# Optimization experiments

Hardware: AMD Instinct MI355X
Metric: run time of the kernel (lower is better)

Reference implementation:

```python
import jax, jax.numpy as jnp
import numpy as np

C = 64  # in_channels == out_channels (required by final view)

def setup_inputs() -> dict:
    key = jax.random.key(0)
    ks = jax.random.split(key, 7)
    x = jax.random.normal(ks[0], (2, C, 16, 16, 16), dtype=jnp.float32)
    s = 1.0 / np.sqrt(C)
    Wq = jax.random.uniform(ks[1], (C, C), jnp.float32, -s, s)
    bq = jax.random.uniform(ks[2], (C,), jnp.float32, -s, s)
    Wk = jax.random.uniform(ks[3], (C, C), jnp.float32, -s, s)
    bk = jax.random.uniform(ks[4], (C,), jnp.float32, -s, s)
    Wv = jax.random.uniform(ks[5], (C, C), jnp.float32, -s, s)
    bv = jax.random.uniform(ks[6], (C,), jnp.float32, -s, s)
    return {"x": x, "Wq": Wq, "bq": bq, "Wk": Wk, "bk": bk, "Wv": Wv, "bv": bv}

def _proj(x, W, b):
    # 1x1x1 Conv3d == per-voxel channel GEMM; x: [B,C,D,H,W]
    return jnp.einsum('oc,bcdhw->bodhw', W, x) + b[None, :, None, None, None]

def reference(x, Wq, bq, Wk, bk, Wv, bv):
    B, Cin, D, H, W = x.shape
    q = _proj(x, Wq, bq).reshape(B, C, -1)  # [B,C,N]
    k = _proj(x, Wk, bk).reshape(B, C, -1)
    v = _proj(x, Wv, bv).reshape(B, C, -1)
    # attention[b,i,j] = softmax_j(q_i . k_j); NOTE: unscaled, as in the source
    attn = jax.nn.softmax(jnp.einsum('bci,bcj->bij', q, k), axis=-1)
    out = jnp.einsum('bcj,bij->bci', v, attn)  # out_i = sum_j a_ij v_j
    return out.reshape(x.shape)
```

## Files before the change

kernel.cpp:

```cpp
#include <hip/hip_runtime.h>
#include <math.h>

#define CCH 64
#define NVOX 4096
#define NB 2
#define RS 72

typedef _Float16 f16x8 __attribute__((ext_vector_type(8)));
typedef float f32x4 __attribute__((ext_vector_type(4)));

__global__ __launch_bounds__(256) void qkv_proj(
    const float* __restrict__ x,
    const float* __restrict__ Wq, const float* __restrict__ bq,
    const float* __restrict__ Wk, const float* __restrict__ bk,
    const float* __restrict__ Wv, const float* __restrict__ bv,
    _Float16* __restrict__ qh, _Float16* __restrict__ kh, _Float16* __restrict__ vh)
{
    __shared__ float Ws[3 * 64 * 64];
    __shared__ float xs[64 * 32];
    const int t  = threadIdx.x;
    const int b  = blockIdx.x >> 7;
    const int i0 = (blockIdx.x & 127) * 32;

    {
        const float4* Wq4 = (const float4*)Wq;
        const float4* Wk4 = (const float4*)Wk;
        const float4* Wv4 = (const float4*)Wv;
        float4* Ws4 = (float4*)Ws;
#pragma unroll
        for (int s = 0; s < 4; ++s) {
            int idx = t + 256 * s;
            Ws4[idx]        = Wq4[idx];
            Ws4[1024 + idx] = Wk4[idx];
            Ws4[2048 + idx] = Wv4[idx];
        }
    }
    {
        int cc = t >> 2;
        int m0 = (t & 3) * 8;
        const float* src = x + ((b * CCH + cc) * NVOX) + i0 + m0;
#pragma unroll
        for (int s = 0; s < 8; ++s) xs[cc * 32 + m0 + s] = src[s];
    }
    __syncthreads();

    const int vox = t & 31;
    const int c0  = (t >> 5) * 8;

#pragma unroll
    for (int m = 0; m < 3; ++m) {
        const float* Wm  = &Ws[m * 4096];
        const float* bia = (m == 0) ? bq : (m == 1) ? bk : bv;
        float acc[8];
#pragma unroll
        for (int j = 0; j < 8; ++j) acc[j] = bia[c0 + j];
        for (int cc = 0; cc < 64; cc += 4) {
            float xv0 = xs[(cc + 0) * 32 + vox];
            float xv1 = xs[(cc + 1) * 32 + vox];
            float xv2 = xs[(cc + 2) * 32 + vox];
            float xv3 = xs[(cc + 3) * 32 + vox];
#pragma unroll
            for (int j = 0; j < 8; ++j) {
                float4 w = *(const float4*)&Wm[(c0 + j) * 64 + cc];
                acc[j] = fmaf(w.x, xv0, acc[j]);
                acc[j] = fmaf(w.y, xv1, acc[j]);
                acc[j] = fmaf(w.z, xv2, acc[j]);
                acc[j] = fmaf(w.w, xv3, acc[j]);
            }
        }
        if (m < 2) {
            f16x8 hv;
#pragma unroll
            for (int j = 0; j < 8; ++j) hv[j] = (_Float16)acc[j];
            _Float16* dst = ((m == 0) ? qh : kh) + ((b * NVOX) + i0 + vox) * CCH + c0;
            *(f16x8*)dst = hv;
        } else {
#pragma unroll
            for (int j = 0; j < 8; ++j)
                vh[(b * CCH + c0 + j) * NVOX + i0 + vox] = (_Float16)acc[j];
        }
    }
}

template <int SPLIT>
__global__ __launch_bounds__(256) void attn(
    const _Float16* __restrict__ qh, const _Float16* __restrict__ kh,
    const _Float16* __restrict__ vh,
    float* __restrict__ po,
    float* __restrict__ ml,
    float* __restrict__ out)
{
    __shared__ _Float16 qs [64 * RS];
    __shared__ _Float16 ksl[64 * RS];
    __shared__ _Float16 vsl[64 * RS];
    __shared__ _Float16 ps [4 * 16 * RS];
    __shared__ float    als[4 * 16];

    constexpr int LS = (SPLIT == 4) ? 2 : (SPLIT == 2) ? 1 : 0;
    const int t    = threadIdx.x;
    const int h    = blockIdx.x & (SPLIT - 1);
    const int tile = blockIdx.x >> LS;
    const int b    = tile >> 6;
    const int i0   = (tile & 63) * 64;

    const int lane = t & 63;
    const int w    = t >> 6;
    const int q4   = lane >> 4;
    const int n    = lane & 15;

    {
        int row = t >> 2, c0 = (t & 3) * 16;
        const float4* src = (const float4*)&qh[((b * NVOX) + i0 + row) * CCH + c0];
        *(float4*)&qs[row * RS + c0]     = src[0];
        *(float4*)&qs[row * RS + c0 + 8] = src[1];
    }

    f16x8 aq[2];
    float m_prev[4], l[4];
    f32x4 o[4];
#pragma unroll
    for (int r = 0; r < 4; ++r) { m_prev[r] = -1e30f; l[r] = 0.f; }
#pragma unroll
    for (int mt = 0; mt < 4; ++mt) o[mt] = (f32x4){0.f, 0.f, 0.f, 0.f};

    const int JT = 64 / SPLIT;
    for (int jt = 0; jt < JT; ++jt) {
        const int j0 = (h * JT + jt) * 64;
        __syncthreads();
        {
            int row = t >> 2, c0 = (t & 3) * 16;
            const float4* ks = (const float4*)&kh[((b * NVOX) + j0 + row) * CCH + c0];
            *(float4*)&ksl[row * RS + c0]     = ks[0];
            *(float4*)&ksl[row * RS + c0 + 8] = ks[1];
            const float4* vs = (const float4*)&vh[(b * CCH + row) * NVOX + j0 + c0];
            *(float4*)&vsl[row * RS + c0]     = vs[0];
            *(float4*)&vsl[row * RS + c0 + 8] = vs[1];
        }
        __syncthreads();

        if (jt == 0) {
#pragma unroll
            for (int ks = 0; ks < 2; ++ks)
                aq[ks] = *(const f16x8*)&qs[(w * 16 + n) * RS + ks * 32 + q4 * 8];
        }

        f32x4 s[4];
#pragma unroll
        for (int nt = 0; nt < 4; ++nt) s[nt] = (f32x4){0.f, 0.f, 0.f, 0.f};
#pragma unroll
        for (int ks = 0; ks < 2; ++ks) {
#pragma unroll
            for (int nt = 0; nt < 4; ++nt) {
                f16x8 bk = *(const f16x8*)&ksl[(nt * 16 + n) * RS + ks * 32 + q4 * 8];
                s[nt] = __builtin_amdgcn_mfma_f32_16x16x32_f16(aq[ks], bk, s[nt], 0, 0, 0);
            }
        }

        float p[4][4], alpha[4];
#pragma unroll
        for (int r = 0; r < 4; ++r) {
            float mx = fmaxf(fmaxf(s[0][r], s[1][r]), fmaxf(s[2][r], s[3][r]));
#pragma unroll
            for (int off = 1; off < 16; off <<= 1)
                mx = fmaxf(mx, __shfl_xor(mx, off, 64));
            float mn = fmaxf(m_prev[r], mx);
            float sum = 0.f;
#pragma unroll
            for (int nt = 0; nt < 4; ++nt) {
                p[nt][r] = __expf(s[nt][r] - mn);
                sum += p[nt][r];
            }
#pragma unroll
            for (int off = 1; off < 16; off <<= 1)
                sum += __shfl_xor(sum, off, 64);
            alpha[r]  = __expf(m_prev[r] - mn);
            l[r]      = l[r] * alpha[r] + sum;
            m_prev[r] = mn;
        }

#pragma unroll
        for (int nt = 0; nt < 4; ++nt)
#pragma unroll
            for (int r = 0; r < 4; ++r)
                ps[w * 16 * RS + (q4 * 4 + r) * RS + nt * 16 + n] = (_Float16)p[nt][r];
        if (n == 0)
            *(float4*)&als[w * 16 + q4 * 4] =
                make_float4(alpha[0], alpha[1], alpha[2], alpha[3]);
        __syncthreads();

        float a_i = als[w * 16 + n];
#pragma unroll
        for (int mt = 0; mt < 4; ++mt)
#pragma unroll
            for (int r = 0; r < 4; ++r) o[mt][r] *= a_i;

        f16x8 bp[2];
#pragma unroll
        for (int ks = 0; ks < 2; ++ks)
            bp[ks] = *(const f16x8*)&ps[w * 16 * RS + n * RS + ks * 32 + q4 * 8];
#pragma unroll
        for (int mt = 0; mt < 4; ++mt) {
#pragma unroll
            for (int ks = 0; ks < 2; ++ks) {
                f16x8 av = *(const f16x8*)&vsl[(mt * 16 + n) * RS + ks * 32 + q4 * 8];
                o[mt] = __builtin_amdgcn_mfma_f32_16x16x32_f16(av, bp[ks], o[mt], 0, 0, 0);
            }
        }
    }

    const int ig = i0 + w * 16 + n;
    if (SPLIT > 1) {
        const size_t base = ((size_t)(b * SPLIT + h) * 64) * NVOX;
#pragma unroll
        for (int mt = 0; mt < 4; ++mt)
#pragma unroll
            for (int r = 0; r < 4; ++r)
                po[base + (size_t)(mt * 16 + q4 * 4 + r) * NVOX + ig] = o[mt][r];
        if (n == 0) {
            const int mlbase = ((b * SPLIT + h) * NVOX + i0 + w * 16 + q4 * 4) * 2;
            *(float4*)&ml[mlbase]     = make_float4(m_prev[0], l[0], m_prev[1], l[1]);
            *(float4*)&ml[mlbase + 4] = make_float4(m_prev[2], l[2], m_prev[3], l[3]);
        }
    } else {
        if (n == 0)
            *(float4*)&als[w * 16 + q4 * 4] =
                make_float4(1.f / l[0], 1.f / l[1], 1.f / l[2], 1.f / l[3]);
        __syncthreads();
        float inv = als[w * 16 + n];
#pragma unroll
        for (int mt = 0; mt < 4; ++mt)
#pragma unroll
            for (int r = 0; r < 4; ++r)
                out[(size_t)(b * CCH + mt * 16 + q4 * 4 + r) * NVOX + ig] = o[mt][r] * inv;
    }
}

template <int SPLIT>
__global__ __launch_bounds__(256) void combine(
    const float* __restrict__ po, const float* __restrict__ ml,
    float* __restrict__ out)
{
    __shared__ float wls[SPLIT * 64];
    const int t  = threadIdx.x;
    const int b  = blockIdx.x >> 6;
    const int i0 = (blockIdx.x & 63) * 64;

    if (t < 64) {
        const int i = i0 + t;
        float mv[SPLIT], lv[SPLIT], M = -1e30f;
#pragma unroll
        for (int h = 0; h < SPLIT; ++h) {
            mv[h] = ml[((b * SPLIT + h) * NVOX + i) * 2 + 0];
            lv[h] = ml[((b * SPLIT + h) * NVOX + i) * 2 + 1];
            M = fmaxf(M, mv[h]);
        }
        float den = 0.f;
#pragma unroll
        for (int h = 0; h < SPLIT; ++h) den += lv[h] * __expf(mv[h] - M);
        const float inv = 1.0f / den;
#pragma unroll
        for (int h = 0; h < SPLIT; ++h) wls[h * 64 + t] = __expf(mv[h] - M) * inv;
    }
    __syncthreads();

    const int c  = t >> 2;
    const int iq = t & 3;
    float4 acc[4];
#pragma unroll
    for (int u = 0; u < 4; ++u) acc[u] = make_float4(0.f, 0.f, 0.f, 0.f);
#pragma unroll
    for (int h = 0; h < SPLIT; ++h) {
        const float4* src = (const float4*)&po[((size_t)(b * SPLIT + h) * 64 + c) * NVOX + i0 + iq * 16];
        const float*  wp  = &wls[h * 64 + iq * 16];
#pragma unroll
        for (int u = 0; u < 4; ++u) {
            float4 f = src[u];
            float4 wv = *(const float4*)&wp[u * 4];
            acc[u].x = fmaf(f.x, wv.x, acc[u].x);
            acc[u].y = fmaf(f.y, wv.y, acc[u].y);
            acc[u].z = fmaf(f.z, wv.z, acc[u].z);
            acc[u].w = fmaf(f.w, wv.w, acc[u].w);
        }
    }
    float4* dst = (float4*)&out[(size_t)(b * CCH + c) * NVOX + i0 + iq * 16];
#pragma unroll
    for (int u = 0; u < 4; ++u) dst[u] = acc[u];
}

extern "C" void kernel_launch(void* const* d_in, const int* in_sizes, int n_in,
                              void* d_out, int out_size, void* d_ws, size_t ws_size,
                              hipStream_t stream)
{
    const float* x  = (const float*)d_in[0];
    const float* Wq = (const float*)d_in[1];
    const float* bq = (const float*)d_in[2];
    const float* Wk = (const float*)d_in[3];
    const float* bk = (const float*)d_in[4];
    const float* Wv = (const float*)d_in[5];
    const float* bv = (const float*)d_in[6];
    float* out = (float*)d_out;

    _Float16* qh = (_Float16*)d_ws;
    _Float16* kh = qh + NB * NVOX * CCH;
    _Float16* vh = kh + NB * NVOX * CCH;
    float*    po = (float*)(vh + NB * NVOX * CCH);
    const size_t qkv_bytes = (size_t)3 * NB * NVOX * CCH * sizeof(_Float16);

    qkv_proj<<<NB * (NVOX / 32), 256, 0, stream>>>(x, Wq, bq, Wk, bk, Wv, bv, qh, kh, vh);

    const size_t need4 = qkv_bytes + (size_t)NB * 4 * (64 + 2) * NVOX * sizeof(float);
    const size_t need2 = qkv_bytes + (size_t)NB * 2 * (64 + 2) * NVOX * sizeof(float);

    if (ws_size >= need4) {
        float* ml = po + (size_t)NB * 4 * 64 * NVOX;
        attn<4><<<NB * 64 * 4, 256, 0, stream>>>(qh, kh, vh, po, ml, out);
        combine<4><<<NB * 64, 256, 0, stream>>>(po, ml, out);
    } else if (ws_size >= need2) {
        float* ml = po + (size_t)NB * 2 * 64 * NVOX;
        attn<2><<<NB * 64 * 2, 256, 0, stream>>>(qh, kh, vh, po, ml, out);
        combine<2><<<NB * 64, 256, 0, stream>>>(po, ml, out);
    } else {
        attn<1><<<NB * 64, 256, 0, stream>>>(qh, kh, vh, nullptr, nullptr, out);
    }
}
```

Before: 118.0 us.

## Transpose QK^T MFMA to keep P in registers and add split-8 path

The score MFMA is swapped to compute S^T, so each lane owns one query column. The softmax row max and sum then need only two cross-lane shuffles, and the probabilities can feed the PV MFMA (16x16x16) straight from registers. This removes the P and alpha shared-memory staging, an extra __syncthreads per tile, and the Q shared-memory staging. A SPLIT=8 variant is also added when the workspace allows, giving more blocks in exchange for more partial-output traffic in combine.

```diff
diff --git a/kernel.cpp b/kernel.cpp
--- a/kernel.cpp
+++ b/kernel.cpp
@@ -7,6 +7,7 @@
 #define RS 72
 
 typedef _Float16 f16x8 __attribute__((ext_vector_type(8)));
+typedef _Float16 f16x4 __attribute__((ext_vector_type(4)));
 typedef float f32x4 __attribute__((ext_vector_type(4)));
 
 __global__ __launch_bounds__(256) void qkv_proj(
@@ -90,13 +91,10 @@
     float* __restrict__ ml,
     float* __restrict__ out)
 {
-    __shared__ _Float16 qs [64 * RS];
     __shared__ _Float16 ksl[64 * RS];
     __shared__ _Float16 vsl[64 * RS];
-    __shared__ _Float16 ps [4 * 16 * RS];
-    __shared__ float    als[4 * 16];
-
-    constexpr int LS = (SPLIT == 4) ? 2 : (SPLIT == 2) ? 1 : 0;
+
+    constexpr int LS = (SPLIT == 8) ? 3 : (SPLIT == 4) ? 2 : (SPLIT == 2) ? 1 : 0;
     const int t    = threadIdx.x;
     const int h    = blockIdx.x & (SPLIT - 1);
     const int tile = blockIdx.x >> LS;
@@ -108,18 +106,15 @@
     const int q4   = lane >> 4;
     const int n    = lane & 15;
 
+    f16x8 aq[2];
     {
-        int row = t >> 2, c0 = (t & 3) * 16;
-        const float4* src = (const float4*)&qh[((b * NVOX) + i0 + row) * CCH + c0];
-        *(float4*)&qs[row * RS + c0]     = src[0];
-        *(float4*)&qs[row * RS + c0 + 8] = src[1];
-    }
-
-    f16x8 aq[2];
-    float m_prev[4], l[4];
+        const _Float16* qrow = qh + ((size_t)(b * NVOX) + i0 + w * 16 + n) * CCH + q4 * 8;
+        aq[0] = *(const f16x8*)(qrow);
+        aq[1] = *(const f16x8*)(qrow + 32);
+    }
+
+    float m_prev = -1e30f, l = 0.f;
     f32x4 o[4];
-#pragma unroll
-    for (int r = 0; r < 4; ++r) { m_prev[r] = -1e30f; l[r] = 0.f; }
 #pragma unroll
     for (int mt = 0; mt < 4; ++mt) o[mt] = (f32x4){0.f, 0.f, 0.f, 0.f};
 
@@ -129,21 +124,15 @@
         __syncthreads();
         {
             int row = t >> 2, c0 = (t & 3) * 16;
-            const float4* ks = (const float4*)&kh[((b * NVOX) + j0 + row) * CCH + c0];
+            const float4* ks = (const float4*)&kh[((size_t)(b * NVOX) + j0 + row) * CCH + c0];
             *(float4*)&ksl[row * RS + c0]     = ks[0];
             *(float4*)&ksl[row * RS + c0 + 8] = ks[1];
-            const float4* vs = (const float4*)&vh[(b * CCH + row) * NVOX + j0 + c0];
+            const float4* vs = (const float4*)&vh[((size_t)b * CCH + row) * NVOX + j0 + c0];
             *(float4*)&vsl[row * RS + c0]     = vs[0];
             *(float4*)&vsl[row * RS + c0 + 8] = vs[1];
         }
         __syncthreads();
 
-        if (jt == 0) {
-#pragma unroll
-            for (int ks = 0; ks < 2; ++ks)
-                aq[ks] = *(const f16x8*)&qs[(w * 16 + n) * RS + ks * 32 + q4 * 8];
-        }
-
         f32x4 s[4];
 #pragma unroll
         for (int nt = 0; nt < 4; ++nt) s[nt] = (f32x4){0.f, 0.f, 0.f, 0.f};
@@ -151,59 +140,52 @@
         for (int ks = 0; ks < 2; ++ks) {
 #pragma unroll
             for (int nt = 0; nt < 4; ++nt) {
-                f16x8 bk = *(const f16x8*)&ksl[(nt * 16 + n) * RS + ks * 32 + q4 * 8];
-                s[nt] = __builtin_amdgcn_mfma_f32_16x16x32_f16(aq[ks], bk, s[nt], 0, 0, 0);
+                f16x8 ak = *(const f16x8*)&ksl[(nt * 16 + n) * RS + ks * 32 + q4 * 8];
+                s[nt] = __builtin_amdgcn_mfma_f32_16x16x32_f16(ak, aq[ks], s[nt], 0, 0, 0);
             }
         }
 
-        float p[4][4], alpha[4];
-#pragma unroll
-        for (int r = 0; r < 4; ++r) {
-            float mx = fmaxf(fmaxf(s[0][r], s[1][r]), fmaxf(s[2][r], s[3][r]));
-#pragma unroll
-            for (int off = 1; off < 16; off <<= 1)
-                mx = fmaxf(mx, __shfl_xor(mx, off, 64));
-            float mn = fmaxf(m_prev[r], mx);
-            float sum = 0.f;
-#pragma unroll
-            for (int nt = 0; nt < 4; ++nt) {
+        float mx = -1e30f;
+#pragma unroll
+        for (int nt = 0; nt < 4; ++nt)
+#pragma unroll
+            for (int r = 0; r < 4; ++r) mx = fmaxf(mx, s[nt][r]);
+        mx = fmaxf(mx, __shfl_xor(mx, 16, 64));
+        mx = fmaxf(mx, __shfl_xor(mx, 32, 64));
+        const float mn = fmaxf(m_prev, mx);
+
+        float p[4][4], sum = 0.f;
+#pragma unroll
+        for (int nt = 0; nt < 4; ++nt)
+#pragma unroll
+            for (int r = 0; r < 4; ++r) {
                 p[nt][r] = __expf(s[nt][r] - mn);
                 sum += p[nt][r];
             }
-#pragma unroll
-            for (int off = 1; off < 16; off <<= 1)
-                sum += __shfl_xor(sum, off, 64);
-            alpha[r]  = __expf(m_prev[r] - mn);
-            l[r]      = l[r] * alpha[r] + sum;
-            m_prev[r] = mn;
-        }
-
+        sum += __shfl_xor(sum, 16, 64);
+        sum += __shfl_xor(sum, 32, 64);
+
+        const float alpha = __expf(m_prev - mn);
+        l = l * alpha + sum;
+        m_prev = mn;
+
+#pragma unroll
+        for (int mt = 0; mt < 4; ++mt)
+#pragma unroll
+            for (int r = 0; r < 4; ++r) o[mt][r] *= alpha;
+
+        f16x4 bp[4];
 #pragma unroll
         for (int nt = 0; nt < 4; ++nt)
 #pragma unroll
-            for (int r = 0; r < 4; ++r)
-                ps[w * 16 * RS + (q4 * 4 + r) * RS + nt * 16 + n] = (_Float16)p[nt][r];
-        if (n == 0)
-            *(float4*)&als[w * 16 + q4 * 4] =
-                make_float4(alpha[0], alpha[1], alpha[2], alpha[3]);
-        __syncthreads();
-
-        float a_i = als[w * 16 + n];
-#pragma unroll
-        for (int mt = 0; mt < 4; ++mt)
-#pragma unroll
-            for (int r = 0; r < 4; ++r) o[mt][r] *= a_i;
-
-        f16x8 bp[2];
-#pragma unroll
-        for (int ks = 0; ks < 2; ++ks)
-            bp[ks] = *(const f16x8*)&ps[w * 16 * RS + n * RS + ks * 32 + q4 * 8];
-#pragma unroll
-        for (int mt = 0; mt < 4; ++mt) {
-#pragma unroll
-            for (int ks = 0; ks < 2; ++ks) {
-                f16x8 av = *(const f16x8*)&vsl[(mt * 16 + n) * RS + ks * 32 + q4 * 8];
-                o[mt] = __builtin_amdgcn_mfma_f32_16x16x32_f16(av, bp[ks], o[mt], 0, 0, 0);
+            for (int r = 0; r < 4; ++r) bp[nt][r] = (_Float16)p[nt][r];
+
+#pragma unroll
+        for (int nt = 0; nt < 4; ++nt) {
+#pragma unroll
+            for (int mt = 0; mt < 4; ++mt) {
+                f16x4 av = *(const f16x4*)&vsl[(mt * 16 + n) * RS + nt * 16 + q4 * 4];
+                o[mt] = __builtin_amdgcn_mfma_f32_16x16x16f16(av, bp[nt], o[mt], 0, 0, 0);
             }
         }
     }
@@ -216,17 +198,12 @@
 #pragma unroll
             for (int r = 0; r < 4; ++r)
                 po[base + (size_t)(mt * 16 + q4 * 4 + r) * NVOX + ig] = o[mt][r];
-        if (n == 0) {
-            const int mlbase = ((b * SPLIT + h) * NVOX + i0 + w * 16 + q4 * 4) * 2;
-            *(float4*)&ml[mlbase]     = make_float4(m_prev[0], l[0], m_prev[1], l[1]);
-            *(float4*)&ml[mlbase + 4] = make_float4(m_prev[2], l[2], m_prev[3], l[3]);
+        if (q4 == 0) {
+            float2* mlp = (float2*)&ml[((size_t)(b * SPLIT + h) * NVOX + ig) * 2];
+            *mlp = make_float2(m_prev, l);
         }
     } else {
-        if (n == 0)
-            *(float4*)&als[w * 16 + q4 * 4] =
-                make_float4(1.f / l[0], 1.f / l[1], 1.f / l[2], 1.f / l[3]);
-        __syncthreads();
-        float inv = als[w * 16 + n];
+        const float inv = 1.0f / l;
 #pragma unroll
         for (int mt = 0; mt < 4; ++mt)
 #pragma unroll
@@ -250,8 +227,8 @@
         float mv[SPLIT], lv[SPLIT], M = -1e30f;
 #pragma unroll
         for (int h = 0; h < SPLIT; ++h) {
-            mv[h] = ml[((b * SPLIT + h) * NVOX + i) * 2 + 0];
-            lv[h] = ml[((b * SPLIT + h) * NVOX + i) * 2 + 1];
+            mv[h] = ml[((size_t)(b * SPLIT + h) * NVOX + i) * 2 + 0];
+            lv[h] = ml[((size_t)(b * SPLIT + h) * NVOX + i) * 2 + 1];
             M = fmaxf(M, mv[h]);
         }
         float den = 0.f;
@@ -308,10 +285,15 @@
 
     qkv_proj<<<NB * (NVOX / 32), 256, 0, stream>>>(x, Wq, bq, Wk, bk, Wv, bv, qh, kh, vh);
 
+    const size_t need8 = qkv_bytes + (size_t)NB * 8 * (64 + 2) * NVOX * sizeof(float);
     const size_t need4 = qkv_bytes + (size_t)NB * 4 * (64 + 2) * NVOX * sizeof(float);
     const size_t need2 = qkv_bytes + (size_t)NB * 2 * (64 + 2) * NVOX * sizeof(float);
 
-    if (ws_size >= need4) {
+    if (ws_size >= need8) {
+        float* ml = po + (size_t)NB * 8 * 64 * NVOX;
+        attn<8><<<NB * 64 * 8, 256, 0, stream>>>(qh, kh, vh, po, ml, out);
+        combine<8><<<NB * 64, 256, 0, stream>>>(po, ml, out);
+    } else if (ws_size >= need4) {
         float* ml = po + (size_t)NB * 4 * 64 * NVOX;
         attn<4><<<NB * 64 * 4, 256, 0, stream>>>(qh, kh, vh, po, ml, out);
         combine<4><<<NB * 64, 256, 0, stream>>>(po, ml, out);
```

Result: faster. 109.8 us (-7.0%).
